# Kernel tuning notes

Measured on AMD Instinct MI355X. Metric: run time of the kernel, lower is better.

## Reference

```python
import jax, jax.numpy as jnp
import numpy as np

N, E = 50000, 1000000
IN_DIM, HID, OUT = 2, 32, 16
H1, H2 = 4, 1
NEG_SLOPE = 0.2
LN_EPS = 1e-5


def _glorot(key, shape):
    fan_in, fan_out = shape[0], shape[1]
    lim = (6.0 / (fan_in + fan_out)) ** 0.5
    return jax.random.uniform(key, shape, jnp.float32, -lim, lim)


def layer_norm(x, g, b):
    mu = jnp.mean(x, axis=-1, keepdims=True)
    var = jnp.var(x, axis=-1, keepdims=True)
    return (x - mu) * jax.lax.rsqrt(var + LN_EPS) * g + b


def gatv2_conv(x, src, dst, edge_attr, Wl, bl, Wr, br, We, att, bias, H, C):
    # x: (N, F) -> out: (N, C)  (concat=False: mean over heads)
    n = x.shape[0]
    xl = (x @ Wl + bl).reshape(n, H, C)   # source transform
    xr = (x @ Wr + br).reshape(n, H, C)   # destination transform
    e = (edge_attr @ We).reshape(-1, H, C)  # edge feature transform (no bias)
    # per-edge message, LeakyReLU, attention logit
    m = jax.nn.leaky_relu(xl[src] + xr[dst] + e, NEG_SLOPE)  # (E, H, C)
    logit = jnp.einsum('ehc,hc->eh', m, att)                 # (E, H)
    # scatter softmax grouped by destination node
    amax = jax.ops.segment_max(logit, dst, num_segments=n)    # (N, H)
    ex = jnp.exp(logit - amax[dst])                           # (E, H)
    denom = jax.ops.segment_sum(ex, dst, num_segments=n)      # (N, H)
    alpha = ex / (denom[dst] + 1e-16)                         # (E, H)
    # weighted scatter-aggregate of source features
    out = jax.ops.segment_sum(alpha[:, :, None] * xl[src], dst, num_segments=n)  # (N, H, C)
    return jnp.mean(out, axis=1) + bias


def setup_inputs() -> dict:
    key = jax.random.key(0)
    ks = jax.random.split(key, 16)
    x = jax.random.normal(ks[0], (N, IN_DIM), jnp.float32)
    edge_index = jax.random.randint(ks[1], (2, E), 0, N, jnp.int64)
    edge_attr = jax.random.normal(ks[2], (E, 1), jnp.float32)
    inp = {
        'x': x, 'edge_index': edge_index, 'edge_attr': edge_attr,
        # layer 1 (in=2 -> H1*HID)
        'W1l': _glorot(ks[3], (IN_DIM, H1 * HID)), 'b1l': jnp.zeros((H1 * HID,), jnp.float32),
        'W1r': _glorot(ks[4], (IN_DIM, H1 * HID)), 'b1r': jnp.zeros((H1 * HID,), jnp.float32),
        'We1': _glorot(ks[5], (1, H1 * HID)),
        'att1': _glorot(ks[6], (H1, HID)),
        'bias1': jnp.zeros((HID,), jnp.float32),
        'g1': jnp.ones((HID,), jnp.float32), 'beta1': jnp.zeros((HID,), jnp.float32),
        # layer 2 (HID -> H2*OUT)
        'W2l': _glorot(ks[7], (HID, H2 * OUT)), 'b2l': jnp.zeros((H2 * OUT,), jnp.float32),
        'W2r': _glorot(ks[8], (HID, H2 * OUT)), 'b2r': jnp.zeros((H2 * OUT,), jnp.float32),
        'We2': _glorot(ks[9], (1, H2 * OUT)),
        'att2': _glorot(ks[10], (H2, OUT)),
        'bias2': jnp.zeros((OUT,), jnp.float32),
        'g2': jnp.ones((OUT,), jnp.float32), 'beta2': jnp.zeros((OUT,), jnp.float32),
    }
    return inp


def reference(x, edge_index, edge_attr, W1l, b1l, W1r, b1r, We1, att1, bias1, g1, beta1,
              W2l, b2l, W2r, b2r, We2, att2, bias2, g2, beta2):
    src, dst = edge_index[0], edge_index[1]
    h = gatv2_conv(x, src, dst, edge_attr, W1l, b1l, W1r, b1r, We1, att1, bias1, H1, HID)
    h = jax.nn.elu(layer_norm(h, g1, beta1))  # dropout p=0.0 -> identity
    z = gatv2_conv(h, src, dst, edge_attr, W2l, b2l, W2r, b2r, We2, att2, bias2, H2, OUT)
    return layer_norm(z, g2, beta2)
```

## Files before the change

kernel.cpp:

```cpp
#include <hip/hip_runtime.h>
#include <hip/hip_bf16.h>
#include <math.h>

typedef __hip_bfloat16 bf16;

__device__ __forceinline__ float b2f(bf16 v) { return __bfloat162float(v); }
__device__ __forceinline__ bf16  f2b(float v) { return __float2bfloat16(v); }

template<int F32>
__device__ __forceinline__ float ldf(const void* p, int i) {
    return F32 ? ((const float*)p)[i] : b2f(((const bf16*)p)[i]);
}
template<int F32>
__device__ __forceinline__ void ldx(const void* x, int s, float& x0, float& x1) {
    if (F32) { float2 v = ((const float2*)x)[s]; x0 = v.x; x1 = v.y; }
    else {
        unsigned u = ((const unsigned*)x)[s];
        x0 = __uint_as_float((u & 0xFFFFu) << 16);
        x1 = __uint_as_float(u & 0xFFFF0000u);
    }
}
__device__ __forceinline__ unsigned f2b_hi(float f) {
    unsigned u = __float_as_uint(f);
    u += 0x7FFFu + ((u >> 16) & 1u);
    return u & 0xFFFF0000u;
}
template<int P4>
__device__ __forceinline__ void ldrec(const void* csr, int k, int& s, float& a) {
    if (P4) {
        unsigned u = ((const unsigned*)csr)[k];
        s = (int)(u & 0xFFFFu);
        a = __uint_as_float(u & 0xFFFF0000u);
    } else {
        uint2 r = ((const uint2*)csr)[k];
        s = (int)r.x;
        a = __uint_as_float(r.y);
    }
}
__device__ __forceinline__ float sclamp(float v, float lim) {
    return fminf(fmaxf(v, -lim), lim);
}
template<int CTRL>
__device__ __forceinline__ float dpp_add(float v) {
    int t = __builtin_amdgcn_update_dpp(0, __float_as_int(v), CTRL, 0xF, 0xF, true);
    return v + __int_as_float(t);
}
__device__ __forceinline__ float red16(float v) {
    v = dpp_add<0xB1>(v);
    v = dpp_add<0x4E>(v);
    v = dpp_add<0x124>(v);
    v = dpp_add<0x128>(v);
    return v;
}

#define NEG_SLOPE 0.2f
#define LN_EPS 1e-5f
#define SCAN_TILE 1024
#define ACHUNK 2048

__device__ __forceinline__ int ld_idx(const int* ei, long long pos, int is64, int N) {
    int v = is64 ? ei[2 * pos] : ei[pos];
    return min(max(v, 0), N - 1);
}
__device__ __forceinline__ int calc_is64(const int* ei) {
    int hi = 0, nz = 0;
    #pragma unroll
    for (int i = 0; i < 8; ++i) { hi |= ei[2 * i + 1]; nz |= ei[2 * i]; }
    return (hi == 0 && nz != 0) ? 1 : 0;
}


__global__ __launch_bounds__(256) void histb_kernel(const int* __restrict__ ei,
                                                    const unsigned short* __restrict__ xu,
                                                    int E, int N, int* __restrict__ flags,
                                                    int* __restrict__ bcnt) {
    __shared__ int c[256];
    int tid = threadIdx.x;
    c[tid] = 0;
    int is64 = calc_is64(ei);
    if (blockIdx.x == 0 && tid == 0) {
        flags[0] = is64;
        int pl = 0;
        for (int i = 0; i < 32; ++i) {
            unsigned ex = (xu[2 * i] >> 7) & 0xFF;
            if (ex >= 100 && ex <= 140) pl++;
        }
        flags[1] = (pl >= 24) ? 0 : 1;
    }
    __syncthreads();
    int i0 = blockIdx.x * ACHUNK;
    int iend = min(i0 + ACHUNK, E);
    for (int i = i0 + tid; i < iend; i += 256)
        atomicAdd(&c[ld_idx(ei, (long long)E + i, is64, N) >> 8], 1);
    __syncthreads();
    if (c[tid]) atomicAdd(&bcnt[tid], c[tid]);
}

__global__ void scanb_kernel(const int* __restrict__ bcnt, int* __restrict__ bbase,
                             int* __restrict__ bcursor, int* __restrict__ rowptr,
                             int N, int E) {
    __shared__ int s[256];
    int tid = threadIdx.x;
    int v = bcnt[tid];
    s[tid] = v;
    __syncthreads();
    for (int off = 1; off < 256; off <<= 1) {
        int u = (tid >= off) ? s[tid - off] : 0;
        __syncthreads();
        s[tid] += u;
        __syncthreads();
    }
    int excl = s[tid] - v;
    bbase[tid] = excl;
    bcursor[tid] = excl;
    if (tid == 255) { bbase[256] = s[255]; rowptr[N] = E; }
}

template<int F32>
__device__ void bina_body(const int* __restrict__ ei, const void* __restrict__ attr,
                          int E, int N, int is64, int* __restrict__ bcursor,
                          uint2* __restrict__ binned) {
    __shared__ int cnt[256], incl[256], cur[256];
    __shared__ uint2 stage[ACHUNK];
    int tid = threadIdx.x;
    cnt[tid] = 0;
    __syncthreads();
    int i0 = blockIdx.x * ACHUNK;
    int iend = min(i0 + ACHUNK, E);
    for (int i = i0 + tid; i < iend; i += 256)
        atomicAdd(&cnt[ld_idx(ei, (long long)E + i, is64, N) >> 8], 1);
    __syncthreads();
    incl[tid] = cnt[tid];
    __syncthreads();
    for (int off = 1; off < 256; off <<= 1) {
        int u = (tid >= off) ? incl[tid - off] : 0;
        __syncthreads();
        incl[tid] += u;
        __syncthreads();
    }
    cur[tid] = incl[tid] - cnt[tid];
    __syncthreads();
    for (int i = i0 + tid; i < iend; i += 256) {
        int d = ld_idx(ei, (long long)E + i, is64, N);
        int s = ld_idx(ei, (long long)i, is64, N);
        float a = ldf<F32>(attr, i);
        int p = atomicAdd(&cur[d >> 8], 1);
        stage[p] = make_uint2((unsigned)s | ((unsigned)(d & 255) << 16), f2b_hi(a));
    }
    __syncthreads();
    int c = cnt[tid];
    if (c > 0) {
        int start = incl[tid] - c;
        int g = atomicAdd(&bcursor[tid], c);
        for (int j = 0; j < c; ++j) binned[g + j] = stage[start + j];
    }
}

__global__ __launch_bounds__(256) void bina_kernel(const int* __restrict__ ei,
                                                   const void* __restrict__ attr,
                                                   int E, int N, const int* __restrict__ flags,
                                                   int* __restrict__ bcursor,
                                                   uint2* __restrict__ binned) {
    if (flags[1]) bina_body<1>(ei, attr, E, N, flags[0], bcursor, binned);
    else          bina_body<0>(ei, attr, E, N, flags[0], bcursor, binned);
}

__global__ __launch_bounds__(256) void passb_kernel(const uint2* __restrict__ binned,
                                                    const int* __restrict__ bbase,
                                                    int* __restrict__ rowptr,
                                                    unsigned* __restrict__ csr, int N) {
    __shared__ int nc[256], incl[256], cur[256];
    int b = blockIdx.x, tid = threadIdx.x;
    int base = bbase[b], cntb = bbase[b + 1] - base;
    nc[tid] = 0;
    __syncthreads();
    for (int i = tid; i < cntb; i += 256)
        atomicAdd(&nc[(binned[base + i].x >> 16) & 255], 1);
    __syncthreads();
    incl[tid] = nc[tid];
    __syncthreads();
    for (int off = 1; off < 256; off <<= 1) {
        int u = (tid >= off) ? incl[tid - off] : 0;
        __syncthreads();
        incl[tid] += u;
        __syncthreads();
    }
    int excl = incl[tid] - nc[tid];
    int node = (b << 8) + tid;
    if (node < N) rowptr[node] = base + excl;
    cur[tid] = excl;
    __syncthreads();
    for (int i = tid; i < cntb; i += 256) {
        uint2 r = binned[base + i];
        int p = atomicAdd(&cur[(r.x >> 16) & 255], 1);
        csr[base + p] = r.y | (r.x & 0xFFFFu);
    }
}


__global__ void hist_kernel(const int* __restrict__ ei, const unsigned short* __restrict__ xu,
                            int E, int N, int* __restrict__ flags, int* __restrict__ cnt) {
    int is64 = calc_is64(ei);
    if (blockIdx.x == 0 && threadIdx.x == 0) {
        flags[0] = is64;
        int pl = 0;
        for (int i = 0; i < 32; ++i) {
            unsigned ex = (xu[2 * i] >> 7) & 0xFF;
            if (ex >= 100 && ex <= 140) pl++;
        }
        flags[1] = (pl >= 24) ? 0 : 1;
    }
    int e = blockIdx.x * blockDim.x + threadIdx.x;
    if (e >= E) return;
    atomicAdd(&cnt[ld_idx(ei, (long long)E + e, is64, N)], 1);
}

__global__ __launch_bounds__(256) void scan_partial(const int* __restrict__ cnt,
                                                    int* __restrict__ bsum, int N) {
    __shared__ int wsum[4];
    int b = blockIdx.x, tid = threadIdx.x;
    int base = b * SCAN_TILE + tid * 4;
    int4 v = make_int4(0, 0, 0, 0);
    if (base + 3 < N) v = *(const int4*)(cnt + base);
    else {
        if (base + 0 < N) v.x = cnt[base + 0];
        if (base + 1 < N) v.y = cnt[base + 1];
        if (base + 2 < N) v.z = cnt[base + 2];
    }
    int s = v.x + v.y + v.z + v.w;
    #pragma unroll
    for (int off = 1; off < 64; off <<= 1) s += __shfl_xor(s, off);
    if ((tid & 63) == 0) wsum[tid >> 6] = s;
    __syncthreads();
    if (tid == 0) bsum[b] = wsum[0] + wsum[1] + wsum[2] + wsum[3];
}

__global__ __launch_bounds__(256) void scan_final(int* __restrict__ cnt, int* __restrict__ rowptr,
                                                  const int* __restrict__ bsum, int N, int B) {
    __shared__ int tsum[256];
    __shared__ int bpre[256];
    int b = blockIdx.x, tid = threadIdx.x;
    bpre[tid] = (tid < B) ? bsum[tid] : 0;
    int base = b * SCAN_TILE + tid * 4;
    int4 v = make_int4(0, 0, 0, 0);
    if (base + 3 < N) v = *(const int4*)(cnt + base);
    else {
        if (base + 0 < N) v.x = cnt[base + 0];
        if (base + 1 < N) v.y = cnt[base + 1];
        if (base + 2 < N) v.z = cnt[base + 2];
    }
    tsum[tid] = v.x + v.y + v.z + v.w;
    __syncthreads();
    for (int off = 1; off < 256; off <<= 1) {
        int t = (tid >= off) ? tsum[tid - off] : 0;
        int u = (tid >= off) ? bpre[tid - off] : 0;
        __syncthreads();
        tsum[tid] += t;
        bpre[tid] += u;
        __syncthreads();
    }
    int blockpre = (b == 0) ? 0 : bpre[b - 1];
    int o0 = blockpre + ((tid == 0) ? 0 : tsum[tid - 1]);
    int o1 = o0 + v.x, o2 = o1 + v.y, o3 = o2 + v.z;
    if (base + 3 < N) {
        int4 o = make_int4(o0, o1, o2, o3);
        *(int4*)(rowptr + base) = o;
        *(int4*)(cnt + base) = o;
    } else {
        if (base + 0 < N) { rowptr[base + 0] = o0; cnt[base + 0] = o0; }
        if (base + 1 < N) { rowptr[base + 1] = o1; cnt[base + 1] = o1; }
        if (base + 2 < N) { rowptr[base + 2] = o2; cnt[base + 2] = o2; }
    }
    if (b == 0 && tid == 255) rowptr[N] = bpre[255];
}

template<int F32>
__device__ void scatter_body(const int* __restrict__ ei, const void* __restrict__ attr,
                             int E, int N, int is64, int* __restrict__ cursor,
                             uint2* __restrict__ csr) {
    int e = blockIdx.x * blockDim.x + threadIdx.x;
    if (e >= E) return;
    int d = ld_idx(ei, (long long)E + e, is64, N);
    int s = ld_idx(ei, (long long)e, is64, N);
    float av = ldf<F32>(attr, e);
    int pos = atomicAdd(&cursor[d], 1);
    csr[pos] = make_uint2((unsigned)s, __float_as_uint(av));
}

__global__ void scatter_kernel(const int* __restrict__ ei, const void* __restrict__ attr,
                               int E, int N, const int* __restrict__ flags,
                               int* __restrict__ cursor, uint2* __restrict__ csr) {
    if (flags[1]) scatter_body<1>(ei, attr, E, N, flags[0], cursor, csr);
    else          scatter_body<0>(ei, attr, E, N, flags[0], cursor, csr);
}


template<int F32, int P4>
__device__ void agg1_body(
    const int* __restrict__ rowptr, const void* __restrict__ csr,
    const void* __restrict__ x,
    const void* W1l, const void* b1l, const void* W1r, const void* b1r,
    const void* We1, const void* att1, const void* bias1, const void* g1v, const void* beta1,
    bf16* __restrict__ hout, int N) {
    int w0 = __builtin_amdgcn_readfirstlane((blockIdx.x * blockDim.x + threadIdx.x) >> 6);
    int NW = (gridDim.x * blockDim.x) >> 6;
    int lane = threadIdx.x & 63;
    int h = lane >> 4, q = lane & 15;
    int ja = h * 32 + q, jb = ja + 16;

    float wlaA = ldf<F32>(W1l, ja),      wlaB = ldf<F32>(W1l, jb);
    float wlbA = ldf<F32>(W1l, 128 + ja), wlbB = ldf<F32>(W1l, 128 + jb);
    float wraA = ldf<F32>(W1r, ja),      wraB = ldf<F32>(W1r, jb);
    float wrbA = ldf<F32>(W1r, 128 + ja), wrbB = ldf<F32>(W1r, 128 + jb);
    float blA = ldf<F32>(b1l, ja), blB = ldf<F32>(b1l, jb);
    float brA = ldf<F32>(b1r, ja), brB = ldf<F32>(b1r, jb);
    float weA = ldf<F32>(We1, ja), weB = ldf<F32>(We1, jb);
    float atA = ldf<F32>(att1, ja), atB = ldf<F32>(att1, jb);
    float aa4A = 0.4f * atA, aa4B = 0.4f * atB;
    float blbrA = blA + brA, blbrB = blB + brB;
    float P0 = 0.6f * red16(atA * wlaA + atB * wlaB);
    float P1 = 0.6f * red16(atA * wlbA + atB * wlbB);
    float Pw = 0.6f * red16(atA * weA + atB * weB);
    float Q0 = 0.6f * red16(atA * wraA + atB * wraB);
    float Q1 = 0.6f * red16(atA * wrbA + atB * wrbB);
    float Qc = 0.6f * red16(atA * blbrA + atB * blbrB);
    float biasA = ldf<F32>(bias1, q), biasB = ldf<F32>(bias1, q + 16);
    float gA = ldf<F32>(g1v, q), gB = ldf<F32>(g1v, q + 16);
    float beA = ldf<F32>(beta1, q), beB = ldf<F32>(beta1, q + 16);

    for (int n = w0; n < N; n += NW) {
        int beg = rowptr[n], end = rowptr[n + 1];
        float xd0, xd1;
        ldx<F32>(x, n, xd0, xd1);
        float cA = fmaf(xd0, wraA, fmaf(xd1, wrbA, blbrA));
        float cB = fmaf(xd0, wraB, fmaf(xd1, wrbB, blbrB));
        float Kn = fmaf(xd0, Q0, fmaf(xd1, Q1, Qc));
        float S = 0.f, Sx0 = 0.f, Sx1 = 0.f;

        auto edge = [&](float xs0, float xs1, float a) {
            float zA = fmaf(xs0, wlaA, fmaf(xs1, wlbA, fmaf(a, weA, cA)));
            float zB = fmaf(xs0, wlaB, fmaf(xs1, wlbB, fmaf(a, weB, cB)));
            float pabs = red16(fmaf(fabsf(zA), aa4A, fabsf(zB) * aa4B));
            float p = sclamp(fmaf(xs0, P0, fmaf(xs1, P1, fmaf(a, Pw, Kn))) + pabs, 60.f);
            float e = __expf(p);
            S += e;
            Sx0 = fmaf(e, xs0, Sx0);
            Sx1 = fmaf(e, xs1, Sx1);
        };

        int k = beg;
        for (; k + 4 <= end; k += 4) {
            int s0, s1, s2, s3;
            float a0, a1, a2, a3;
            ldrec<P4>(csr, k, s0, a0);
            ldrec<P4>(csr, k + 1, s1, a1);
            ldrec<P4>(csr, k + 2, s2, a2);
            ldrec<P4>(csr, k + 3, s3, a3);
            float p0, p1, q0, q1, r0, r1, t0, t1;
            ldx<F32>(x, s0, p0, p1);
            ldx<F32>(x, s1, q0, q1);
            ldx<F32>(x, s2, r0, r1);
            ldx<F32>(x, s3, t0, t1);
            edge(p0, p1, a0);
            edge(q0, q1, a1);
            edge(r0, r1, a2);
            edge(t0, t1, a3);
        }
        for (; k < end; ++k) {
            int s0; float a0;
            ldrec<P4>(csr, k, s0, a0);
            float p0, p1;
            ldx<F32>(x, s0, p0, p1);
            edge(p0, p1, a0);
        }

        float inv = 1.0f / (S + 1e-16f);
        float R = S * inv, U0 = Sx0 * inv, U1 = Sx1 * inv;
        float outA = fmaf(U0, wlaA, fmaf(U1, wlbA, R * blA));
        float outB = fmaf(U0, wlaB, fmaf(U1, wlbB, R * blB));
        outA += __shfl_xor(outA, 16); outA += __shfl_xor(outA, 32);
        outB += __shfl_xor(outB, 16); outB += __shfl_xor(outB, 32);
        float valA = fmaf(0.25f, outA, biasA);
        float valB = fmaf(0.25f, outB, biasB);
        float mu = red16(valA + valB) * (1.f / 32.f);
        float dA = valA - mu, dB = valB - mu;
        float var = red16(dA * dA + dB * dB) * (1.f / 32.f);
        float rs = rsqrtf(var + LN_EPS);
        float yA = fmaf(dA * rs, gA, beA);
        float yB = fmaf(dB * rs, gB, beB);
        float hA = yA > 0.f ? yA : expm1f(yA);
        float hB = yB > 0.f ? yB : expm1f(yB);
        if (lane < 16) {
            hout[n * 32 + q]      = f2b(hA);
            hout[n * 32 + 16 + q] = f2b(hB);
        }
    }
}

template<int P4>
__global__ __launch_bounds__(256) void agg1_kernel(
    const int* __restrict__ flags,
    const int* __restrict__ rowptr, const void* __restrict__ csr,
    const void* __restrict__ x,
    const void* W1l, const void* b1l, const void* W1r, const void* b1r,
    const void* We1, const void* att1, const void* bias1, const void* g1v, const void* beta1,
    bf16* __restrict__ hout, int N) {
    if (flags[1]) agg1_body<1, P4>(rowptr, csr, x, W1l, b1l, W1r, b1r,
                                   We1, att1, bias1, g1v, beta1, hout, N);
    else          agg1_body<0, P4>(rowptr, csr, x, W1l, b1l, W1r, b1r,
                                   We1, att1, bias1, g1v, beta1, hout, N);
}


template<int F32>
__device__ void node2_body(bf16* __restrict__ hbuf, float* wl, float* wr,
                           const void* W2l, const void* b2l, const void* W2r, const void* b2r,
                           int N) {
    __shared__ float bl[16], br[16];
    int tid = threadIdx.x;
    for (int i = tid; i < 512; i += 256) { wl[i] = ldf<F32>(W2l, i); wr[i] = ldf<F32>(W2r, i); }
    if (tid < 16) { bl[tid] = ldf<F32>(b2l, tid); br[tid] = ldf<F32>(b2r, tid); }
    __syncthreads();
    int n = blockIdx.x * blockDim.x + tid;
    if (n >= N) return;
    float hv[32];
    #pragma unroll
    for (int c = 0; c < 32; ++c) hv[c] = b2f(hbuf[n * 32 + c]);
    float accl[16], accr[16];
    #pragma unroll
    for (int o = 0; o < 16; ++o) { accl[o] = bl[o]; accr[o] = br[o]; }
    #pragma unroll
    for (int c = 0; c < 32; ++c) {
        #pragma unroll
        for (int o = 0; o < 16; ++o) {
            accl[o] = fmaf(hv[c], wl[c * 16 + o], accl[o]);
            accr[o] = fmaf(hv[c], wr[c * 16 + o], accr[o]);
        }
    }
    #pragma unroll
    for (int o = 0; o < 16; ++o) {
        hbuf[n * 32 + o]      = f2b(accl[o]);
        hbuf[n * 32 + 16 + o] = f2b(accr[o]);
    }
}

__global__ __launch_bounds__(256) void node2_kernel(
    const int* __restrict__ flags, bf16* __restrict__ hbuf,
    const void* W2l, const void* b2l, const void* W2r, const void* b2r, int N) {
    __shared__ float wl[512], wr[512];
    if (flags[1]) node2_body<1>(hbuf, wl, wr, W2l, b2l, W2r, b2r, N);
    else          node2_body<0>(hbuf, wl, wr, W2l, b2l, W2r, b2r, N);
}


template<int F32, int P4>
__device__ void agg2_body(
    const int* __restrict__ rowptr, const void* __restrict__ csr,
    const bf16* __restrict__ h2,
    const void* We2, const void* att2, const void* bias2, const void* g2v, const void* beta2,
    void* __restrict__ out, int N) {
    int w0 = __builtin_amdgcn_readfirstlane((blockIdx.x * blockDim.x + threadIdx.x) >> 6);
    int NW = (gridDim.x * blockDim.x) >> 6;
    int lane = threadIdx.x & 63;
    int g = lane >> 4, t = lane & 15;

    float we = ldf<F32>(We2, t), at = ldf<F32>(att2, t);
    float bia = ldf<F32>(bias2, t), gg = ldf<F32>(g2v, t), bb = ldf<F32>(beta2, t);

    for (int n = w0; n < N; n += NW) {
        int beg = rowptr[n], end = rowptr[n + 1];
        float xr = b2f(h2[n * 32 + 16 + t]);

        float S = 0.f, A = 0.f;
        auto edge = [&](float v, float a) {
            float m = fmaf(a, we, v + xr);
            m = fmaxf(m, NEG_SLOPE * m);
            float p = sclamp(red16(m * at), 60.f);
            float e = __expf(p);
            S += e;
            A = fmaf(e, v, A);
        };
        int k = beg + g;
        for (; k + 4 < end; k += 8) {
            int s0, s1; float a0, a1;
            ldrec<P4>(csr, k, s0, a0);
            ldrec<P4>(csr, k + 4, s1, a1);
            float v0 = b2f(h2[s0 * 32 + t]);
            float v1 = b2f(h2[s1 * 32 + t]);
            edge(v0, a0);
            edge(v1, a1);
        }
        if (k < end) {
            int s0; float a0;
            ldrec<P4>(csr, k, s0, a0);
            edge(b2f(h2[s0 * 32 + t]), a0);
        }
        S += __shfl_xor(S, 16); S += __shfl_xor(S, 32);
        A += __shfl_xor(A, 16); A += __shfl_xor(A, 32);
        float val = A / (S + 1e-16f) + bia;

        float mu = red16(val) * (1.f / 16.f);
        float d = val - mu;
        float var = red16(d * d) * (1.f / 16.f);
        float y = fmaf(d * rsqrtf(var + LN_EPS), gg, bb);
        if (lane < 16) {
            if (F32) ((float*)out)[n * 16 + t] = y;
            else     ((bf16*)out)[n * 16 + t] = f2b(y);
        }
    }
}

template<int P4>
__global__ __launch_bounds__(256) void agg2_kernel(
    const int* __restrict__ flags,
    const int* __restrict__ rowptr, const void* __restrict__ csr,
    const bf16* __restrict__ h2,
    const void* We2, const void* att2, const void* bias2, const void* g2v, const void* beta2,
    void* __restrict__ out, int N) {
    if (flags[1]) agg2_body<1, P4>(rowptr, csr, h2, We2, att2, bias2, g2v, beta2, out, N);
    else          agg2_body<0, P4>(rowptr, csr, h2, We2, att2, bias2, g2v, beta2, out, N);
}


static inline size_t align256(size_t x) { return (x + 255) & ~size_t(255); }

extern "C" void kernel_launch(void* const* d_in, const int* in_sizes, int n_in,
                              void* d_out, int out_size, void* d_ws, size_t ws_size,
                              hipStream_t stream) {
    const void* x     = d_in[0];
    const int*  ei    = (const int*)d_in[1];
    const void* eattr = d_in[2];
    const void* W1l   = d_in[3];
    const void* b1l   = d_in[4];
    const void* W1r   = d_in[5];
    const void* b1r   = d_in[6];
    const void* We1   = d_in[7];
    const void* att1  = d_in[8];
    const void* bias1 = d_in[9];
    const void* g1    = d_in[10];
    const void* beta1 = d_in[11];
    const void* W2l   = d_in[12];
    const void* b2l   = d_in[13];
    const void* W2r   = d_in[14];
    const void* b2r   = d_in[15];
    const void* We2   = d_in[16];
    const void* att2  = d_in[17];
    const void* bias2 = d_in[18];
    const void* g2    = d_in[19];
    const void* beta2 = d_in[20];

    const int N = in_sizes[0] / 2;
    const int E = in_sizes[2];
    const bool p4 = (N <= 65536);
    const int EB = (E + ACHUNK - 1) / ACHUNK;

    char* ws = (char*)d_ws;
    size_t off = 0;
    int* flags   = (int*)(ws + off); off += align256(sizeof(int) * 2);
    int* bcnt    = (int*)(ws + off); off += align256(sizeof(int) * 1024);
    int* bbase   = (int*)(ws + off); off += align256(sizeof(int) * 257);
    int* bcursor = (int*)(ws + off); off += align256(sizeof(int) * 256);
    int* rowptr  = (int*)(ws + off); off += align256(sizeof(int) * (size_t)(N + 1));
    void* csr    = (void*)(ws + off); off += align256((p4 ? 4u : 8u) * (size_t)E);
    char* big    = (ws + off);
    uint2* binned = (uint2*)big;
    int*   cnt    = (int*)big;
    bf16*  hbuf   = (bf16*)big;

    if (p4) {
        hipMemsetAsync(bcnt, 0, sizeof(int) * 256, stream);
        histb_kernel<<<EB, 256, 0, stream>>>(ei, (const unsigned short*)x, E, N, flags, bcnt);
        scanb_kernel<<<1, 256, 0, stream>>>(bcnt, bbase, bcursor, rowptr, N, E);
        bina_kernel<<<EB, 256, 0, stream>>>(ei, eattr, E, N, flags, bcursor, binned);
        passb_kernel<<<(N + 255) >> 8, 256, 0, stream>>>(binned, bbase, rowptr, (unsigned*)csr, N);
    } else {
        cnt = (int*)big;
        hbuf = (bf16*)(big + align256(sizeof(int) * (size_t)N));
        const int B = (N + SCAN_TILE - 1) / SCAN_TILE;
        hipMemsetAsync(cnt, 0, sizeof(int) * (size_t)N, stream);
        hist_kernel<<<(E + 255) / 256, 256, 0, stream>>>(ei, (const unsigned short*)x, E, N, flags, cnt);
        scan_partial<<<B, 256, 0, stream>>>(cnt, bcnt, N);
        scan_final<<<B, 256, 0, stream>>>(cnt, rowptr, bcnt, N, B);
        scatter_kernel<<<(E + 255) / 256, 256, 0, stream>>>(ei, eattr, E, N, flags, cnt, (uint2*)csr);
    }

    if (p4) agg1_kernel<1><<<2048, 256, 0, stream>>>(flags, rowptr, csr, x,
                                                     W1l, b1l, W1r, b1r, We1, att1,
                                                     bias1, g1, beta1, hbuf, N);
    else    agg1_kernel<0><<<2048, 256, 0, stream>>>(flags, rowptr, csr, x,
                                                     W1l, b1l, W1r, b1r, We1, att1,
                                                     bias1, g1, beta1, hbuf, N);

    node2_kernel<<<(N + 255) / 256, 256, 0, stream>>>(flags, hbuf, W2l, b2l, W2r, b2r, N);

    if (p4) agg2_kernel<1><<<2048, 256, 0, stream>>>(flags, rowptr, csr, hbuf,
                                                     We2, att2, bias2, g2, beta2, d_out, N);
    else    agg2_kernel<0><<<2048, 256, 0, stream>>>(flags, rowptr, csr, hbuf,
                                                     We2, att2, bias2, g2, beta2, d_out, N);
}
```

Measured before the change: 226.9 us.

## Replace global-cursor binning with per-chunk sorted tiles and per-bucket gather

The CSR build drops the separate histogram pass and the memset. Each chunk block now reads its edges once, sorts them locally by 256-node bucket in shared memory, and writes the tile contiguously along with per-chunk bucket counts and offsets. A small reduction kernel and a scan then compute bucket bases. The per-bucket pass gathers its pieces from every chunk, which removes the global atomic cursor and the edge_index re-read. The cost is serial per-thread loops over up to EB chunks in passb, with short strided reads that may be poorly coalesced.

```diff
diff --git a/kernel.cpp b/kernel.cpp
--- a/kernel.cpp
+++ b/kernel.cpp
@@ -57,6 +57,7 @@
 #define LN_EPS 1e-5f
 #define SCAN_TILE 1024
 #define ACHUNK 2048
+#define EBMAX 512
 
 __device__ __forceinline__ int ld_idx(const int* ei, long long pos, int is64, int N) {
     int v = is64 ? ei[2 * pos] : ei[pos];
@@ -68,40 +69,107 @@
     for (int i = 0; i < 8; ++i) { hi |= ei[2 * i + 1]; nz |= ei[2 * i]; }
     return (hi == 0 && nz != 0) ? 1 : 0;
 }
-
-
-__global__ __launch_bounds__(256) void histb_kernel(const int* __restrict__ ei,
+__device__ __forceinline__ int calc_isf32(const unsigned short* xu) {
+    int pl = 0;
+    for (int i = 0; i < 32; ++i) {
+        unsigned ex = (xu[2 * i] >> 7) & 0xFF;
+        if (ex >= 100 && ex <= 140) pl++;
+    }
+    return (pl >= 24) ? 0 : 1;
+}
+
+
+template<int F32>
+__device__ void bina1_body(const int* __restrict__ ei, const void* __restrict__ attr,
+                           int E, int N, int is64,
+                           uint2* __restrict__ binned, int* __restrict__ cntm,
+                           int* __restrict__ locm,
+                           int* cnt, int* incl, int* cur, uint2* stage) {
+    int tid = threadIdx.x, b = blockIdx.x;
+    cnt[tid] = 0;
+    __syncthreads();
+    int i0 = b * ACHUNK;
+    int iend = min(i0 + ACHUNK, E);
+    uint2 rec[8]; int bk[8];
+    #pragma unroll
+    for (int r = 0; r < 8; ++r) {
+        int i = i0 + tid + r * 256;
+        bk[r] = -1;
+        if (i < iend) {
+            int d = ld_idx(ei, (long long)E + i, is64, N);
+            int s = ld_idx(ei, (long long)i, is64, N);
+            float a = ldf<F32>(attr, i);
+            rec[r] = make_uint2((unsigned)s | ((unsigned)(d & 255) << 16), f2b_hi(a));
+            bk[r] = d >> 8;
+            atomicAdd(&cnt[bk[r]], 1);
+        }
+    }
+    __syncthreads();
+    incl[tid] = cnt[tid];
+    __syncthreads();
+    for (int off = 1; off < 256; off <<= 1) {
+        int u = (tid >= off) ? incl[tid - off] : 0;
+        __syncthreads();
+        incl[tid] += u;
+        __syncthreads();
+    }
+    cur[tid] = incl[tid] - cnt[tid];
+    __syncthreads();
+    #pragma unroll
+    for (int r = 0; r < 8; ++r) {
+        if (bk[r] >= 0) {
+            int p = atomicAdd(&cur[bk[r]], 1);
+            stage[p] = rec[r];
+        }
+    }
+    __syncthreads();
+    int n = iend - i0;
+    for (int i = tid; i < n; i += 256)
+        binned[(size_t)b * ACHUNK + i] = stage[i];
+    cntm[b * 256 + tid] = cnt[tid];
+    locm[b * 256 + tid] = incl[tid] - cnt[tid];
+}
+
+__global__ __launch_bounds__(256) void bina1_kernel(const int* __restrict__ ei,
+                                                    const void* __restrict__ attr,
                                                     const unsigned short* __restrict__ xu,
                                                     int E, int N, int* __restrict__ flags,
-                                                    int* __restrict__ bcnt) {
-    __shared__ int c[256];
-    int tid = threadIdx.x;
-    c[tid] = 0;
-    int is64 = calc_is64(ei);
-    if (blockIdx.x == 0 && tid == 0) {
-        flags[0] = is64;
-        int pl = 0;
-        for (int i = 0; i < 32; ++i) {
-            unsigned ex = (xu[2 * i] >> 7) & 0xFF;
-            if (ex >= 100 && ex <= 140) pl++;
-        }
-        flags[1] = (pl >= 24) ? 0 : 1;
-    }
-    __syncthreads();
-    int i0 = blockIdx.x * ACHUNK;
-    int iend = min(i0 + ACHUNK, E);
-    for (int i = i0 + tid; i < iend; i += 256)
-        atomicAdd(&c[ld_idx(ei, (long long)E + i, is64, N) >> 8], 1);
-    __syncthreads();
-    if (c[tid]) atomicAdd(&bcnt[tid], c[tid]);
-}
-
-__global__ void scanb_kernel(const int* __restrict__ bcnt, int* __restrict__ bbase,
-                             int* __restrict__ bcursor, int* __restrict__ rowptr,
-                             int N, int E) {
+                                                    uint2* __restrict__ binned,
+                                                    int* __restrict__ cntm,
+                                                    int* __restrict__ locm) {
+    __shared__ int cnt[256], incl[256], cur[256];
+    __shared__ uint2 stage[ACHUNK];
+    __shared__ int sflags[2];
+    if (threadIdx.x == 0) {
+        sflags[0] = calc_is64(ei);
+        sflags[1] = calc_isf32(xu);
+        if (blockIdx.x == 0) { flags[0] = sflags[0]; flags[1] = sflags[1]; }
+    }
+    __syncthreads();
+    if (sflags[1]) bina1_body<1>(ei, attr, E, N, sflags[0], binned, cntm, locm,
+                                 cnt, incl, cur, stage);
+    else           bina1_body<0>(ei, attr, E, N, sflags[0], binned, cntm, locm,
+                                 cnt, incl, cur, stage);
+}
+
+__global__ __launch_bounds__(256) void sumb_kernel(const int* __restrict__ cntm,
+                                                   int* __restrict__ btot, int EB) {
+    __shared__ int w[4];
+    int B = blockIdx.x, tid = threadIdx.x;
+    int s = 0;
+    for (int j = tid; j < EB; j += 256) s += cntm[j * 256 + B];
+    #pragma unroll
+    for (int off = 1; off < 64; off <<= 1) s += __shfl_xor(s, off);
+    if ((tid & 63) == 0) w[tid >> 6] = s;
+    __syncthreads();
+    if (tid == 0) btot[B] = w[0] + w[1] + w[2] + w[3];
+}
+
+__global__ void scanc_kernel(const int* __restrict__ btot, int* __restrict__ bbase,
+                             int* __restrict__ rowptr, int NB, int N, int E) {
     __shared__ int s[256];
     int tid = threadIdx.x;
-    int v = bcnt[tid];
+    int v = (tid < NB) ? btot[tid] : 0;
     s[tid] = v;
     __syncthreads();
     for (int off = 1; off < 256; off <<= 1) {
@@ -110,27 +178,34 @@
         s[tid] += u;
         __syncthreads();
     }
-    int excl = s[tid] - v;
-    bbase[tid] = excl;
-    bcursor[tid] = excl;
-    if (tid == 255) { bbase[256] = s[255]; rowptr[N] = E; }
-}
-
-template<int F32>
-__device__ void bina_body(const int* __restrict__ ei, const void* __restrict__ attr,
-                          int E, int N, int is64, int* __restrict__ bcursor,
-                          uint2* __restrict__ binned) {
-    __shared__ int cnt[256], incl[256], cur[256];
-    __shared__ uint2 stage[ACHUNK];
-    int tid = threadIdx.x;
-    cnt[tid] = 0;
-    __syncthreads();
-    int i0 = blockIdx.x * ACHUNK;
-    int iend = min(i0 + ACHUNK, E);
-    for (int i = i0 + tid; i < iend; i += 256)
-        atomicAdd(&cnt[ld_idx(ei, (long long)E + i, is64, N) >> 8], 1);
-    __syncthreads();
-    incl[tid] = cnt[tid];
+    if (tid < NB) bbase[tid] = s[tid] - v;
+    if (tid == 0) { bbase[NB] = s[255]; rowptr[N] = E; }
+}
+
+__global__ __launch_bounds__(256) void passb_kernel(const uint2* __restrict__ binned,
+                                                    const int* __restrict__ cntm,
+                                                    const int* __restrict__ locm,
+                                                    const int* __restrict__ bbase,
+                                                    int* __restrict__ rowptr,
+                                                    unsigned* __restrict__ csr,
+                                                    int N, int EB) {
+    __shared__ int nc[256], incl[256], cur[256];
+    __shared__ int cntl[EBMAX], locl[EBMAX];
+    int B = blockIdx.x, tid = threadIdx.x;
+    for (int j = tid; j < EB; j += 256) {
+        cntl[j] = cntm[j * 256 + B];
+        locl[j] = locm[j * 256 + B];
+    }
+    nc[tid] = 0;
+    __syncthreads();
+    for (int j = tid; j < EB; j += 256) {
+        int c = cntl[j];
+        const uint2* src = binned + (size_t)j * ACHUNK + locl[j];
+        for (int i = 0; i < c; ++i)
+            atomicAdd(&nc[(src[i].x >> 16) & 255], 1);
+    }
+    __syncthreads();
+    incl[tid] = nc[tid];
     __syncthreads();
     for (int off = 1; off < 256; off <<= 1) {
         int u = (tid >= off) ? incl[tid - off] : 0;
@@ -138,62 +213,20 @@
         incl[tid] += u;
         __syncthreads();
     }
-    cur[tid] = incl[tid] - cnt[tid];
-    __syncthreads();
-    for (int i = i0 + tid; i < iend; i += 256) {
-        int d = ld_idx(ei, (long long)E + i, is64, N);
-        int s = ld_idx(ei, (long long)i, is64, N);
-        float a = ldf<F32>(attr, i);
-        int p = atomicAdd(&cur[d >> 8], 1);
-        stage[p] = make_uint2((unsigned)s | ((unsigned)(d & 255) << 16), f2b_hi(a));
-    }
-    __syncthreads();
-    int c = cnt[tid];
-    if (c > 0) {
-        int start = incl[tid] - c;
-        int g = atomicAdd(&bcursor[tid], c);
-        for (int j = 0; j < c; ++j) binned[g + j] = stage[start + j];
-    }
-}
-
-__global__ __launch_bounds__(256) void bina_kernel(const int* __restrict__ ei,
-                                                   const void* __restrict__ attr,
-                                                   int E, int N, const int* __restrict__ flags,
-                                                   int* __restrict__ bcursor,
-                                                   uint2* __restrict__ binned) {
-    if (flags[1]) bina_body<1>(ei, attr, E, N, flags[0], bcursor, binned);
-    else          bina_body<0>(ei, attr, E, N, flags[0], bcursor, binned);
-}
-
-__global__ __launch_bounds__(256) void passb_kernel(const uint2* __restrict__ binned,
-                                                    const int* __restrict__ bbase,
-                                                    int* __restrict__ rowptr,
-                                                    unsigned* __restrict__ csr, int N) {
-    __shared__ int nc[256], incl[256], cur[256];
-    int b = blockIdx.x, tid = threadIdx.x;
-    int base = bbase[b], cntb = bbase[b + 1] - base;
-    nc[tid] = 0;
-    __syncthreads();
-    for (int i = tid; i < cntb; i += 256)
-        atomicAdd(&nc[(binned[base + i].x >> 16) & 255], 1);
-    __syncthreads();
-    incl[tid] = nc[tid];
-    __syncthreads();
-    for (int off = 1; off < 256; off <<= 1) {
-        int u = (tid >= off) ? incl[tid - off] : 0;
-        __syncthreads();
-        incl[tid] += u;
-        __syncthreads();
-    }
+    int base = bbase[B];
     int excl = incl[tid] - nc[tid];
-    int node = (b << 8) + tid;
+    int node = (B << 8) + tid;
     if (node < N) rowptr[node] = base + excl;
     cur[tid] = excl;
     __syncthreads();
-    for (int i = tid; i < cntb; i += 256) {
-        uint2 r = binned[base + i];
-        int p = atomicAdd(&cur[(r.x >> 16) & 255], 1);
-        csr[base + p] = r.y | (r.x & 0xFFFFu);
+    for (int j = tid; j < EB; j += 256) {
+        int c = cntl[j];
+        const uint2* src = binned + (size_t)j * ACHUNK + locl[j];
+        for (int i = 0; i < c; ++i) {
+            uint2 r = src[i];
+            int p = atomicAdd(&cur[(r.x >> 16) & 255], 1);
+            csr[base + p] = r.y | (r.x & 0xFFFFu);
+        }
     }
 }
 
@@ -203,12 +236,7 @@
     int is64 = calc_is64(ei);
     if (blockIdx.x == 0 && threadIdx.x == 0) {
         flags[0] = is64;
-        int pl = 0;
-        for (int i = 0; i < 32; ++i) {
-            unsigned ex = (xu[2 * i] >> 7) & 0xFF;
-            if (ex >= 100 && ex <= 140) pl++;
-        }
-        flags[1] = (pl >= 24) ? 0 : 1;
+        flags[1] = calc_isf32(xu);
     }
     int e = blockIdx.x * blockDim.x + threadIdx.x;
     if (e >= E) return;
@@ -551,36 +579,38 @@
 
     const int N = in_sizes[0] / 2;
     const int E = in_sizes[2];
-    const bool p4 = (N <= 65536);
     const int EB = (E + ACHUNK - 1) / ACHUNK;
+    const int NB = (N + 255) >> 8;
+    const bool p4 = (N <= 65536) && (EB <= EBMAX);
 
     char* ws = (char*)d_ws;
     size_t off = 0;
-    int* flags   = (int*)(ws + off); off += align256(sizeof(int) * 2);
-    int* bcnt    = (int*)(ws + off); off += align256(sizeof(int) * 1024);
-    int* bbase   = (int*)(ws + off); off += align256(sizeof(int) * 257);
-    int* bcursor = (int*)(ws + off); off += align256(sizeof(int) * 256);
-    int* rowptr  = (int*)(ws + off); off += align256(sizeof(int) * (size_t)(N + 1));
-    void* csr    = (void*)(ws + off); off += align256((p4 ? 4u : 8u) * (size_t)E);
-    char* big    = (ws + off);
+    int* flags  = (int*)(ws + off); off += align256(sizeof(int) * 2);
+    int* cntm   = (int*)(ws + off); off += align256(sizeof(int) * (size_t)EB * 256);
+    int* locm   = (int*)(ws + off); off += align256(sizeof(int) * (size_t)EB * 256);
+    int* btot   = (int*)(ws + off); off += align256(sizeof(int) * 256);
+    int* bbase  = (int*)(ws + off); off += align256(sizeof(int) * 257);
+    int* rowptr = (int*)(ws + off); off += align256(sizeof(int) * (size_t)(N + 1));
+    void* csr   = (void*)(ws + off); off += align256((p4 ? 4u : 8u) * (size_t)E);
+    char* big   = (ws + off);
     uint2* binned = (uint2*)big;
-    int*   cnt    = (int*)big;
     bf16*  hbuf   = (bf16*)big;
 
     if (p4) {
-        hipMemsetAsync(bcnt, 0, sizeof(int) * 256, stream);
-        histb_kernel<<<EB, 256, 0, stream>>>(ei, (const unsigned short*)x, E, N, flags, bcnt);
-        scanb_kernel<<<1, 256, 0, stream>>>(bcnt, bbase, bcursor, rowptr, N, E);
-        bina_kernel<<<EB, 256, 0, stream>>>(ei, eattr, E, N, flags, bcursor, binned);
-        passb_kernel<<<(N + 255) >> 8, 256, 0, stream>>>(binned, bbase, rowptr, (unsigned*)csr, N);
+        bina1_kernel<<<EB, 256, 0, stream>>>(ei, eattr, (const unsigned short*)x,
+                                             E, N, flags, binned, cntm, locm);
+        sumb_kernel<<<NB, 256, 0, stream>>>(cntm, btot, EB);
+        scanc_kernel<<<1, 256, 0, stream>>>(btot, bbase, rowptr, NB, N, E);
+        passb_kernel<<<NB, 256, 0, stream>>>(binned, cntm, locm, bbase, rowptr,
+                                             (unsigned*)csr, N, EB);
     } else {
-        cnt = (int*)big;
+        int* cnt = (int*)big;
         hbuf = (bf16*)(big + align256(sizeof(int) * (size_t)N));
         const int B = (N + SCAN_TILE - 1) / SCAN_TILE;
         hipMemsetAsync(cnt, 0, sizeof(int) * (size_t)N, stream);
         hist_kernel<<<(E + 255) / 256, 256, 0, stream>>>(ei, (const unsigned short*)x, E, N, flags, cnt);
-        scan_partial<<<B, 256, 0, stream>>>(cnt, bcnt, N);
-        scan_final<<<B, 256, 0, stream>>>(cnt, rowptr, bcnt, N, B);
+        scan_partial<<<B, 256, 0, stream>>>(cnt, cntm, N);
+        scan_final<<<B, 256, 0, stream>>>(cnt, rowptr, cntm, N, B);
         scatter_kernel<<<(E + 255) / 256, 256, 0, stream>>>(ei, eattr, E, N, flags, cnt, (uint2*)csr);
     }
 
```

Result: faster. 219.0 us (-3.5%).
